# Optimization experiments

Hardware: AMD Instinct MI355X
Metric: run time of the kernel (lower is better)

Reference implementation:

```python
import jax, jax.numpy as jnp
import numpy as np
from jax import lax

DIM = 384
NE = 8
TOPK = 2
HID = 4 * DIM
N, H, W = 32, 32, 32
EPS = 1e-6


def setup_inputs() -> dict:
    key = jax.random.key(0)
    ks = jax.random.split(key, 12)
    s = 0.02
    return {
        "input": jax.random.normal(ks[0], (N, DIM, H, W), dtype=jnp.float32),
        "dw_w": jax.random.normal(ks[1], (DIM, 1, 7, 7), dtype=jnp.float32) * s,
        "dw_b": jnp.zeros((DIM,), dtype=jnp.float32),
        "ln_g": jnp.ones((DIM,), dtype=jnp.float32),
        "ln_b": jnp.zeros((DIM,), dtype=jnp.float32),
        "gate_w": jax.random.normal(ks[2], (NE, DIM), dtype=jnp.float32) * s,
        "w1": jax.random.normal(ks[3], (NE, DIM, HID), dtype=jnp.float32) * s,
        "b1": jnp.zeros((NE, HID), dtype=jnp.float32),
        "w2": jax.random.normal(ks[4], (NE, HID, DIM), dtype=jnp.float32) * s,
        "b2": jnp.zeros((NE, DIM), dtype=jnp.float32),
        "layer_scale": jnp.ones((DIM, 1, 1), dtype=jnp.float32) * 1e-6,
    }


def reference(input, dw_w, dw_b, ln_g, ln_b, gate_w, w1, b1, w2, b2, layer_scale):
    # depthwise 7x7 conv, padding 3, groups=DIM  (NCHW)
    x = lax.conv_general_dilated(
        input, dw_w, window_strides=(1, 1), padding=((3, 3), (3, 3)),
        dimension_numbers=("NCHW", "OIHW", "NCHW"), feature_group_count=DIM,
    ) + dw_b[None, :, None, None]
    # permute to NHWC, layernorm over C with eps=1e-6
    x = jnp.transpose(x, (0, 2, 3, 1))
    mu = jnp.mean(x, axis=-1, keepdims=True)
    var = jnp.mean(jnp.square(x - mu), axis=-1, keepdims=True)
    x = (x - mu) * lax.rsqrt(var + EPS) * ln_g + ln_b

    x_flat = x.reshape(-1, DIM)  # [T, C]
    logits = x_flat @ gate_w.T   # [T, NE]
    topv, topi = lax.top_k(logits, TOPK)
    weights = jax.nn.softmax(topv, axis=-1)  # [T, K]

    # combine: out[t] = sum_e gate_e[t] * Expert_e(x_flat[t]), gate nonzero only for top-k
    out = jnp.zeros_like(x_flat)
    for e in range(NE):
        we = jnp.sum(jnp.where(topi == e, weights, 0.0), axis=-1)  # [T]
        h = jax.nn.gelu(x_flat @ w1[e] + b1[e], approximate=False)
        y = h @ w2[e] + b2[e]
        out = out + y * we[:, None]

    out = out.reshape(N, H, W, DIM)
    out = jnp.transpose(out, (0, 3, 1, 2))  # back to NCHW
    out = layer_scale[None] * out           # [C,1,1] broadcast
    # stochastic_depth prob 0.0 -> identity
    return input + out
```

## Files before the change

### kernel.cpp

```cpp
#include <hip/hip_runtime.h>
#include <hip/hip_bf16.h>
#include <hip/hip_fp8.h>

typedef __attribute__((ext_vector_type(4))) float  f32x4;
typedef __attribute__((ext_vector_type(8))) unsigned short u16x8;
typedef __attribute__((ext_vector_type(4))) unsigned short u16x4;
typedef long long f8x8;

#define DIM 384
#define NE 8
#define HID 1536
#define NB 32
#define HW 1024
#define T_TOK 32768

__device__ __forceinline__ unsigned short f2bf(float f) {
    unsigned int u = __float_as_uint(f);
    u = (u + 0x7fffu + ((u >> 16) & 1u)) >> 16;
    return (unsigned short)u;
}
__device__ __forceinline__ float bf2f(unsigned short u) {
    return __uint_as_float((unsigned int)u << 16);
}
__device__ __forceinline__ unsigned char f2fp8(float f) {
    __hip_fp8_e4m3 h(f);
    return (unsigned char)h.__x;
}

__global__ __launch_bounds__(256) void k_transpose8(const float* __restrict__ src,
                                                    unsigned char* __restrict__ dst,
                                                    int R, int C) {
    int b = blockIdx.x;
    int ctiles = C >> 5;
    int rtiles = R >> 5;
    int ct = b % ctiles;
    int rt = (b / ctiles) % rtiles;
    int e  = b / (ctiles * rtiles);
    __shared__ float t[32][33];
    int tid = threadIdx.x;
    const float* s = src + (size_t)e * R * C;
    unsigned char* d = dst + (size_t)e * C * R;
#pragma unroll
    for (int k = 0; k < 4; ++k) {
        int idx = k * 256 + tid;
        int rr = idx >> 5, cc = idx & 31;
        t[rr][cc] = s[(size_t)(rt * 32 + rr) * C + ct * 32 + cc];
    }
    __syncthreads();
    int cc = tid >> 3, r4 = tid & 7;
    unsigned int pk = 0;
#pragma unroll
    for (int i = 0; i < 4; ++i)
        pk |= (unsigned int)f2fp8(t[r4 * 4 + i][cc]) << (8 * i);
    *(unsigned int*)&d[(size_t)(ct * 32 + cc) * R + rt * 32 + r4 * 4] = pk;
}

__global__ __launch_bounds__(256) void k_conv(const float* __restrict__ in,
                                              const float* __restrict__ dw_w,
                                              const float* __restrict__ dw_b,
                                              float* __restrict__ xconv) {
    int nc = blockIdx.x;
    int c = nc % DIM;
    __shared__ float tile[38 * 38];
    __shared__ float wt[49];
    const float* plane = in + (size_t)nc * HW;
    int tid = threadIdx.x;
    if (tid < 49) wt[tid] = dw_w[c * 49 + tid];
    for (int idx = tid; idx < 38 * 38; idx += 256) {
        int ty = idx / 38, tx = idx % 38;
        int ih = ty - 3, iw = tx - 3;
        float v = 0.f;
        if ((unsigned)ih < 32u && (unsigned)iw < 32u) v = plane[ih * 32 + iw];
        tile[idx] = v;
    }
    __syncthreads();
    float bias = dw_b[c];
    int w = tid & 31, h0 = (tid >> 5) << 2;
    float acc[4] = {bias, bias, bias, bias};
#pragma unroll
    for (int iy = 0; iy < 10; ++iy) {
        float r[7];
#pragma unroll
        for (int dx = 0; dx < 7; ++dx) r[dx] = tile[(h0 + iy) * 38 + w + dx];
#pragma unroll
        for (int o = 0; o < 4; ++o) {
            int dy = iy - o;
            if (dy >= 0 && dy < 7) {
                float a = 0.f;
#pragma unroll
                for (int dx = 0; dx < 7; ++dx) a += r[dx] * wt[dy * 7 + dx];
                acc[o] += a;
            }
        }
    }
    float* outp = xconv + (size_t)nc * HW;
#pragma unroll
    for (int o = 0; o < 4; ++o) outp[(h0 + o) * 32 + w] = acc[o];
}

__global__ __launch_bounds__(256) void k_ln_gate(const float* __restrict__ xconv,
                                                 const float* __restrict__ ln_g,
                                                 const float* __restrict__ ln_b,
                                                 const float* __restrict__ gate_w,
                                                 unsigned char* __restrict__ lnout,
                                                 int* __restrict__ lists,
                                                 float* __restrict__ wgts,
                                                 int* __restrict__ counts) {
    __shared__ float xs[32][385];
    __shared__ float gw[8][384];
    __shared__ float gls[384], bls[384];
    __shared__ int hcnt[8], hbase[8];
    __shared__ int lexp[32][2];
    __shared__ int lpos[32][2];
    __shared__ float lw[32][2];

    int b = blockIdx.x;
    int n = b >> 5;
    int hw0 = (b & 31) << 5;
    int tid = threadIdx.x;

    for (int i = tid; i < 384; i += 256) { gls[i] = ln_g[i]; bls[i] = ln_b[i]; }
    for (int i = tid; i < 8 * 384; i += 256) gw[i / 384][i % 384] = gate_w[i];
    if (tid < 8) hcnt[tid] = 0;

    const float* base = xconv + (size_t)n * DIM * HW + hw0;
#pragma unroll
    for (int k = 0; k < 48; ++k) {
        int idx = k * 256 + tid;
        int c = idx >> 5, j = idx & 31;
        xs[j][c] = base[(size_t)c * HW + j];
    }
    __syncthreads();

    int tok = tid >> 3, jj = tid & 7;
    float sum = 0.f, sq = 0.f;
#pragma unroll
    for (int k = 0; k < 48; ++k) {
        float v = xs[tok][jj + 8 * k];
        sum += v; sq += v * v;
    }
#pragma unroll
    for (int m = 1; m < 8; m <<= 1) { sum += __shfl_xor(sum, m); sq += __shfl_xor(sq, m); }
    float mu = sum * (1.f / 384.f);
    float var = sq * (1.f / 384.f) - mu * mu;
    float rstd = rsqrtf(var + 1e-6f);

    int tglob = n * HW + hw0 + tok;
    float p[8] = {0, 0, 0, 0, 0, 0, 0, 0};
#pragma unroll
    for (int k = 0; k < 48; ++k) {
        int c = jj + 8 * k;
        float v = (xs[tok][c] - mu) * rstd * gls[c] + bls[c];
        lnout[(size_t)tglob * DIM + c] = f2fp8(v);
#pragma unroll
        for (int e = 0; e < 8; ++e) p[e] += v * gw[e][c];
    }
#pragma unroll
    for (int e = 0; e < 8; ++e)
#pragma unroll
        for (int m = 1; m < 8; m <<= 1) p[e] += __shfl_xor(p[e], m);

    if (jj == 0) {
        int i0 = 0; float v0 = p[0];
#pragma unroll
        for (int e = 1; e < 8; ++e) if (p[e] > v0) { v0 = p[e]; i0 = e; }
        int i1 = -1; float v1 = -1e30f;
#pragma unroll
        for (int e = 0; e < 8; ++e) if (e != i0 && p[e] > v1) { v1 = p[e]; i1 = e; }
        float w0 = 1.f / (1.f + __expf(v1 - v0));
        float w1 = 1.f - w0;
        lexp[tok][0] = i0; lexp[tok][1] = i1;
        lw[tok][0] = w0;  lw[tok][1] = w1;
        lpos[tok][0] = atomicAdd(&hcnt[i0], 1);
        lpos[tok][1] = atomicAdd(&hcnt[i1], 1);
    }
    __syncthreads();
    if (tid < 8) hbase[tid] = atomicAdd(&counts[tid], hcnt[tid]);
    __syncthreads();
    if (jj == 0) {
#pragma unroll
        for (int s = 0; s < 2; ++s) {
            int e = lexp[tok][s];
            int pos = hbase[e] + lpos[tok][s];
            lists[e * T_TOK + pos] = (tglob << 1) | s;
            wgts[e * T_TOK + pos] = lw[tok][s];
        }
    }
}

__global__ __launch_bounds__(256, 3) void k_moe(const unsigned char* __restrict__ ln,
                                                const unsigned char* __restrict__ w1t,
                                                const unsigned char* __restrict__ w2t,
                                                const float* __restrict__ b1,
                                                const float* __restrict__ b2,
                                                const int* __restrict__ lists,
                                                const float* __restrict__ wgts,
                                                const int* __restrict__ counts,
                                                unsigned short* __restrict__ y0,
                                                unsigned short* __restrict__ y1) {
    int e    = blockIdx.x & 7;
    int tile = blockIdx.x >> 3;
    int cnt = counts[e];
    if (tile * 64 >= cnt) return;

    __shared__ unsigned char X[64][400];
    __shared__ unsigned char Hs[2][64][136];
    __shared__ int   ents[64];
    __shared__ float wrow[64];

    int tid = threadIdx.x;
    if (tid < 64) {
        int idx = tile * 64 + tid;
        if (idx < cnt) { ents[tid] = lists[e * T_TOK + idx]; wrow[tid] = wgts[e * T_TOK + idx]; }
        else           { ents[tid] = -1;                     wrow[tid] = 0.f; }
    }
    __syncthreads();

    {
        int row = tid >> 2, q = tid & 3;
        int ent = ents[row];
        int tok = (ent < 0) ? 0 : (ent >> 1);
        const u16x8* src = (const u16x8*)(ln + (size_t)tok * DIM);
#pragma unroll
        for (int r = 0; r < 6; ++r)
            *(u16x8*)&X[row][(q + r * 4) * 16] = __builtin_nontemporal_load(&src[q + r * 4]);
    }
    __syncthreads();

    int wid = tid >> 6;
    int lane = tid & 63;
    int lr = lane & 15;
    int lq = lane >> 4;

    const unsigned char* pw1 = w1t + ((size_t)e * HID + wid * 32 + lr) * DIM + lq * 8;
    const unsigned char* pw2 = w2t + ((size_t)e * DIM + wid * 96 + lr) * HID + lq * 8;

    f32x4 Yacc[6][4] = {};

    for (int hc = 0; hc < 12; ++hc) {
        int buf = hc & 1;
        const unsigned char* q1 = pw1 + (size_t)hc * 128 * DIM;
        f32x4 bv0 = *(const f32x4*)&b1[e * HID + hc * 128 + wid * 32 + lq * 4];
        f32x4 bv1 = *(const f32x4*)&b1[e * HID + hc * 128 + wid * 32 + 16 + lq * 4];
        f32x4 Hf[4][2];
#pragma unroll
        for (int m = 0; m < 4; ++m) { Hf[m][0] = bv0; Hf[m][1] = bv1; }
        __builtin_amdgcn_s_setprio(1);
#pragma unroll
        for (int k = 0; k < 12; ++k) {
            f8x8 w0 = *(const f8x8*)(q1 + k * 32);
            f8x8 w1f = *(const f8x8*)(q1 + 16 * DIM + k * 32);
            f8x8 a0 = *(const f8x8*)&X[ 0 + lr][k * 32 + lq * 8];
            f8x8 a1 = *(const f8x8*)&X[16 + lr][k * 32 + lq * 8];
            f8x8 a2 = *(const f8x8*)&X[32 + lr][k * 32 + lq * 8];
            f8x8 a3 = *(const f8x8*)&X[48 + lr][k * 32 + lq * 8];
            Hf[0][0] = __builtin_amdgcn_mfma_f32_16x16x32_fp8_fp8(w0, a0, Hf[0][0], 0, 0, 0);
            Hf[1][0] = __builtin_amdgcn_mfma_f32_16x16x32_fp8_fp8(w0, a1, Hf[1][0], 0, 0, 0);
            Hf[2][0] = __builtin_amdgcn_mfma_f32_16x16x32_fp8_fp8(w0, a2, Hf[2][0], 0, 0, 0);
            Hf[3][0] = __builtin_amdgcn_mfma_f32_16x16x32_fp8_fp8(w0, a3, Hf[3][0], 0, 0, 0);
            Hf[0][1] = __builtin_amdgcn_mfma_f32_16x16x32_fp8_fp8(w1f, a0, Hf[0][1], 0, 0, 0);
            Hf[1][1] = __builtin_amdgcn_mfma_f32_16x16x32_fp8_fp8(w1f, a1, Hf[1][1], 0, 0, 0);
            Hf[2][1] = __builtin_amdgcn_mfma_f32_16x16x32_fp8_fp8(w1f, a2, Hf[2][1], 0, 0, 0);
            Hf[3][1] = __builtin_amdgcn_mfma_f32_16x16x32_fp8_fp8(w1f, a3, Hf[3][1], 0, 0, 0);
        }
        __builtin_amdgcn_s_setprio(0);
#pragma unroll
        for (int nj = 0; nj < 2; ++nj) {
#pragma unroll
            for (int m = 0; m < 4; ++m) {
                unsigned int pk = 0;
#pragma unroll
                for (int r = 0; r < 4; ++r) {
                    float v = Hf[m][nj][r];
                    float zz = v * fmaf(v * v, -0.07135481627f, -1.5957691216f);
                    float g = v * __builtin_amdgcn_rcpf(1.f + __expf(zz));
                    pk |= (unsigned int)f2fp8(g) << (8 * r);
                }
                *(unsigned int*)&Hs[buf][m * 16 + lr][wid * 32 + nj * 16 + lq * 4] = pk;
            }
        }
        asm volatile("s_waitcnt lgkmcnt(0)" ::: "memory");
        __builtin_amdgcn_s_barrier();
        __builtin_amdgcn_sched_barrier(0);
        const unsigned char* q2 = pw2 + hc * 128;
        __builtin_amdgcn_s_setprio(1);
#pragma unroll
        for (int k2 = 0; k2 < 4; ++k2) {
            f8x8 h0 = *(const f8x8*)&Hs[buf][ 0 + lr][k2 * 32 + lq * 8];
            f8x8 h1 = *(const f8x8*)&Hs[buf][16 + lr][k2 * 32 + lq * 8];
            f8x8 h2 = *(const f8x8*)&Hs[buf][32 + lr][k2 * 32 + lq * 8];
            f8x8 h3 = *(const f8x8*)&Hs[buf][48 + lr][k2 * 32 + lq * 8];
#pragma unroll
            for (int nj = 0; nj < 6; ++nj) {
                f8x8 wf = *(const f8x8*)(q2 + (size_t)nj * 16 * HID + k2 * 32);
                Yacc[nj][0] = __builtin_amdgcn_mfma_f32_16x16x32_fp8_fp8(wf, h0, Yacc[nj][0], 0, 0, 0);
                Yacc[nj][1] = __builtin_amdgcn_mfma_f32_16x16x32_fp8_fp8(wf, h1, Yacc[nj][1], 0, 0, 0);
                Yacc[nj][2] = __builtin_amdgcn_mfma_f32_16x16x32_fp8_fp8(wf, h2, Yacc[nj][2], 0, 0, 0);
                Yacc[nj][3] = __builtin_amdgcn_mfma_f32_16x16x32_fp8_fp8(wf, h3, Yacc[nj][3], 0, 0, 0);
            }
        }
        __builtin_amdgcn_s_setprio(0);
    }

    f32x4 b2v[6];
#pragma unroll
    for (int nj = 0; nj < 6; ++nj)
        b2v[nj] = *(const f32x4*)&b2[e * DIM + wid * 96 + nj * 16 + lq * 4];
#pragma unroll
    for (int m = 0; m < 4; ++m) {
        int row = m * 16 + lr;
        int ent = ents[row];
        if (ent >= 0) {
            float wv = wrow[row];
            int tok = ent >> 1;
            unsigned short* yb = (ent & 1) ? y1 : y0;
#pragma unroll
            for (int nj = 0; nj < 6; ++nj) {
                u16x4 pk;
#pragma unroll
                for (int r = 0; r < 4; ++r)
                    pk[r] = f2bf((Yacc[nj][m][r] + b2v[nj][r]) * wv);
                *(u16x4*)(yb + (size_t)tok * DIM + wid * 96 + nj * 16 + lq * 4) = pk;
            }
        }
    }
}

__global__ __launch_bounds__(256) void k_final(const float* __restrict__ input,
                                               const float* __restrict__ ls,
                                               const unsigned short* __restrict__ y0,
                                               const unsigned short* __restrict__ y1,
                                               float* __restrict__ out) {
    int b = blockIdx.x;
    int ct = b % 12;
    int hwt = (b / 12) % 32;
    int n = b / (12 * 32);
    int c0 = ct * 32, hw0 = hwt * 32;
    __shared__ float t[32][33];
    int tid = threadIdx.x;
    int t0 = n * HW + hw0;
#pragma unroll
    for (int k = 0; k < 2; ++k) {
        int idx = k * 256 + tid;
        int tl = idx >> 4, pr = idx & 15;
        size_t o = (size_t)(t0 + tl) * DIM + c0 + pr * 2;
        unsigned int a = *(const unsigned int*)(y0 + o);
        unsigned int c = *(const unsigned int*)(y1 + o);
        t[tl][pr * 2]     = bf2f((unsigned short)a) + bf2f((unsigned short)c);
        t[tl][pr * 2 + 1] = bf2f((unsigned short)(a >> 16)) + bf2f((unsigned short)(c >> 16));
    }
    __syncthreads();
#pragma unroll
    for (int k = 0; k < 4; ++k) {
        int idx = k * 256 + tid;
        int cl = idx >> 5, j = idx & 31;
        size_t o = ((size_t)n * DIM + c0 + cl) * HW + hw0 + j;
        out[o] = input[o] + ls[c0 + cl] * t[j][cl];
    }
}

extern "C" void kernel_launch(void* const* d_in, const int* in_sizes, int n_in,
                              void* d_out, int out_size, void* d_ws, size_t ws_size,
                              hipStream_t stream) {
    const float* input  = (const float*)d_in[0];
    const float* dw_w   = (const float*)d_in[1];
    const float* dw_b   = (const float*)d_in[2];
    const float* ln_g   = (const float*)d_in[3];
    const float* ln_b   = (const float*)d_in[4];
    const float* gate_w = (const float*)d_in[5];
    const float* w1     = (const float*)d_in[6];
    const float* b1     = (const float*)d_in[7];
    const float* w2     = (const float*)d_in[8];
    const float* b2     = (const float*)d_in[9];
    const float* lscale = (const float*)d_in[10];

    const size_t SZ_PLANE = (size_t)NB * DIM * HW * 4;
    const size_t SZ_YBF   = (size_t)T_TOK * DIM * 2;
    const size_t SZ_LNB   = (size_t)T_TOK * DIM;
    const size_t SZ_W1    = (size_t)NE * DIM * HID;
    char* ws = (char*)d_ws;
    float* xconv = (float*)(ws + 0);
    unsigned short* y0 = (unsigned short*)(ws + 0);
    unsigned short* y1 = (unsigned short*)(ws + SZ_YBF);
    unsigned char* lnb = (unsigned char*)(ws + SZ_PLANE);
    unsigned char* w1t = (unsigned char*)(ws + SZ_PLANE + SZ_LNB);
    unsigned char* w2t = (unsigned char*)(ws + SZ_PLANE + SZ_LNB + SZ_W1);
    int*   lists  = (int*)(ws + SZ_PLANE + SZ_LNB + 2 * SZ_W1);
    float* wgt    = (float*)(ws + SZ_PLANE + SZ_LNB + 2 * SZ_W1 + 1048576);
    int*   counts = (int*)(ws + SZ_PLANE + SZ_LNB + 2 * SZ_W1 + 2 * 1048576);
    const size_t needed = SZ_PLANE + SZ_LNB + 2 * SZ_W1 + 2 * 1048576 + 256;
    if (ws_size < needed) return;

    hipMemsetAsync(counts, 0, 32, stream);
    k_transpose8<<<8 * 12 * 48, 256, 0, stream>>>(w1, w1t, DIM, HID);
    k_transpose8<<<8 * 48 * 12, 256, 0, stream>>>(w2, w2t, HID, DIM);
    k_conv<<<NB * DIM, 256, 0, stream>>>(input, dw_w, dw_b, xconv);
    k_ln_gate<<<T_TOK / 32, 256, 0, stream>>>(xconv, ln_g, ln_b, gate_w, lnb, lists, wgt, counts);
    k_moe<<<NE * 512, 256, 0, stream>>>(lnb, w1t, w2t, b1, b2, lists, wgt, counts, y0, y1);
    k_final<<<NB * 32 * 12, 256, 0, stream>>>(input, lscale, y0, y1, (float*)d_out);
}
```

Measured before the change: 485.2 us.

## Restructure MoE kernel into larger hidden chunks with register-prefetched W1 fragments

The MoE kernel now walks the hidden dimension in 4 chunks of 384 instead of 12 chunks of 128. Each wave computes three 32-column slices per chunk with all 12 K-steps of W1 fragments preloaded into registers, and a single enlarged H buffer replaces the double buffer, which adds a second barrier per chunk. This cuts the barrier count and lengthens the second GEMM's inner loop, but raises register use, so launch bounds drop from 3 to 2 blocks per CU. FP8 packing also switches to the hardware packed-convert builtin where available.

```diff
diff --git a/kernel.cpp b/kernel.cpp
--- a/kernel.cpp
+++ b/kernel.cpp
@@ -25,6 +25,20 @@
 __device__ __forceinline__ unsigned char f2fp8(float f) {
     __hip_fp8_e4m3 h(f);
     return (unsigned char)h.__x;
+}
+__device__ __forceinline__ float gelu_f(float v) {
+    float zz = v * fmaf(v * v, -0.07135481627f, -1.5957691216f);
+    return v * __builtin_amdgcn_rcpf(1.f + __expf(zz));
+}
+__device__ __forceinline__ unsigned int pk4_fp8(float a, float b, float c, float d) {
+#if __has_builtin(__builtin_amdgcn_cvt_pk_fp8_f32)
+    int v = __builtin_amdgcn_cvt_pk_fp8_f32(a, b, 0, false);
+    v = __builtin_amdgcn_cvt_pk_fp8_f32(c, d, v, true);
+    return (unsigned int)v;
+#else
+    return (unsigned int)f2fp8(a) | ((unsigned int)f2fp8(b) << 8) |
+           ((unsigned int)f2fp8(c) << 16) | ((unsigned int)f2fp8(d) << 24);
+#endif
 }
 
 __global__ __launch_bounds__(256) void k_transpose8(const float* __restrict__ src,
@@ -48,10 +62,8 @@
     }
     __syncthreads();
     int cc = tid >> 3, r4 = tid & 7;
-    unsigned int pk = 0;
-#pragma unroll
-    for (int i = 0; i < 4; ++i)
-        pk |= (unsigned int)f2fp8(t[r4 * 4 + i][cc]) << (8 * i);
+    unsigned int pk = pk4_fp8(t[r4 * 4 + 0][cc], t[r4 * 4 + 1][cc],
+                              t[r4 * 4 + 2][cc], t[r4 * 4 + 3][cc]);
     *(unsigned int*)&d[(size_t)(ct * 32 + cc) * R + rt * 32 + r4 * 4] = pk;
 }
 
@@ -188,7 +200,7 @@
     }
 }
 
-__global__ __launch_bounds__(256, 3) void k_moe(const unsigned char* __restrict__ ln,
+__global__ __launch_bounds__(256, 2) void k_moe(const unsigned char* __restrict__ ln,
                                                 const unsigned char* __restrict__ w1t,
                                                 const unsigned char* __restrict__ w2t,
                                                 const float* __restrict__ b1,
@@ -204,7 +216,7 @@
     if (tile * 64 >= cnt) return;
 
     __shared__ unsigned char X[64][400];
-    __shared__ unsigned char Hs[2][64][136];
+    __shared__ unsigned char Hs[64][392];
     __shared__ int   ents[64];
     __shared__ float wrow[64];
 
@@ -227,69 +239,69 @@
     }
     __syncthreads();
 
-    int wid = tid >> 6;
+    int w    = tid >> 6;
     int lane = tid & 63;
     int lr = lane & 15;
     int lq = lane >> 4;
 
-    const unsigned char* pw1 = w1t + ((size_t)e * HID + wid * 32 + lr) * DIM + lq * 8;
-    const unsigned char* pw2 = w2t + ((size_t)e * DIM + wid * 96 + lr) * HID + lq * 8;
-
     f32x4 Yacc[6][4] = {};
 
-    for (int hc = 0; hc < 12; ++hc) {
-        int buf = hc & 1;
-        const unsigned char* q1 = pw1 + (size_t)hc * 128 * DIM;
-        f32x4 bv0 = *(const f32x4*)&b1[e * HID + hc * 128 + wid * 32 + lq * 4];
-        f32x4 bv1 = *(const f32x4*)&b1[e * HID + hc * 128 + wid * 32 + 16 + lq * 4];
-        f32x4 Hf[4][2];
-#pragma unroll
-        for (int m = 0; m < 4; ++m) { Hf[m][0] = bv0; Hf[m][1] = bv1; }
+    for (int hc = 0; hc < 4; ++hc) {
         __builtin_amdgcn_s_setprio(1);
 #pragma unroll
-        for (int k = 0; k < 12; ++k) {
-            f8x8 w0 = *(const f8x8*)(q1 + k * 32);
-            f8x8 w1f = *(const f8x8*)(q1 + 16 * DIM + k * 32);
-            f8x8 a0 = *(const f8x8*)&X[ 0 + lr][k * 32 + lq * 8];
-            f8x8 a1 = *(const f8x8*)&X[16 + lr][k * 32 + lq * 8];
-            f8x8 a2 = *(const f8x8*)&X[32 + lr][k * 32 + lq * 8];
-            f8x8 a3 = *(const f8x8*)&X[48 + lr][k * 32 + lq * 8];
-            Hf[0][0] = __builtin_amdgcn_mfma_f32_16x16x32_fp8_fp8(w0, a0, Hf[0][0], 0, 0, 0);
-            Hf[1][0] = __builtin_amdgcn_mfma_f32_16x16x32_fp8_fp8(w0, a1, Hf[1][0], 0, 0, 0);
-            Hf[2][0] = __builtin_amdgcn_mfma_f32_16x16x32_fp8_fp8(w0, a2, Hf[2][0], 0, 0, 0);
-            Hf[3][0] = __builtin_amdgcn_mfma_f32_16x16x32_fp8_fp8(w0, a3, Hf[3][0], 0, 0, 0);
-            Hf[0][1] = __builtin_amdgcn_mfma_f32_16x16x32_fp8_fp8(w1f, a0, Hf[0][1], 0, 0, 0);
-            Hf[1][1] = __builtin_amdgcn_mfma_f32_16x16x32_fp8_fp8(w1f, a1, Hf[1][1], 0, 0, 0);
-            Hf[2][1] = __builtin_amdgcn_mfma_f32_16x16x32_fp8_fp8(w1f, a2, Hf[2][1], 0, 0, 0);
-            Hf[3][1] = __builtin_amdgcn_mfma_f32_16x16x32_fp8_fp8(w1f, a3, Hf[3][1], 0, 0, 0);
+        for (int s = 0; s < 3; ++s) {
+            int hb = hc * 384 + w * 96 + s * 32;
+            const unsigned char* pa = w1t + ((size_t)e * HID + hb + lr) * DIM + lq * 8;
+            f8x8 wa[2][12];
+#pragma unroll
+            for (int nj = 0; nj < 2; ++nj)
+#pragma unroll
+                for (int k = 0; k < 12; ++k)
+                    wa[nj][k] = *(const f8x8*)(pa + (size_t)nj * 16 * DIM + k * 32);
+            f32x4 bv0 = *(const f32x4*)&b1[e * HID + hb + lq * 4];
+            f32x4 bv1 = *(const f32x4*)&b1[e * HID + hb + 16 + lq * 4];
+            f32x4 Hacc[2][4];
+#pragma unroll
+            for (int m = 0; m < 4; ++m) { Hacc[0][m] = bv0; Hacc[1][m] = bv1; }
+#pragma unroll
+            for (int k = 0; k < 12; ++k) {
+                f8x8 a0 = *(const f8x8*)&X[ 0 + lr][k * 32 + lq * 8];
+                f8x8 a1 = *(const f8x8*)&X[16 + lr][k * 32 + lq * 8];
+                f8x8 a2 = *(const f8x8*)&X[32 + lr][k * 32 + lq * 8];
+                f8x8 a3 = *(const f8x8*)&X[48 + lr][k * 32 + lq * 8];
+                Hacc[0][0] = __builtin_amdgcn_mfma_f32_16x16x32_fp8_fp8(wa[0][k], a0, Hacc[0][0], 0, 0, 0);
+                Hacc[0][1] = __builtin_amdgcn_mfma_f32_16x16x32_fp8_fp8(wa[0][k], a1, Hacc[0][1], 0, 0, 0);
+                Hacc[0][2] = __builtin_amdgcn_mfma_f32_16x16x32_fp8_fp8(wa[0][k], a2, Hacc[0][2], 0, 0, 0);
+                Hacc[0][3] = __builtin_amdgcn_mfma_f32_16x16x32_fp8_fp8(wa[0][k], a3, Hacc[0][3], 0, 0, 0);
+                Hacc[1][0] = __builtin_amdgcn_mfma_f32_16x16x32_fp8_fp8(wa[1][k], a0, Hacc[1][0], 0, 0, 0);
+                Hacc[1][1] = __builtin_amdgcn_mfma_f32_16x16x32_fp8_fp8(wa[1][k], a1, Hacc[1][1], 0, 0, 0);
+                Hacc[1][2] = __builtin_amdgcn_mfma_f32_16x16x32_fp8_fp8(wa[1][k], a2, Hacc[1][2], 0, 0, 0);
+                Hacc[1][3] = __builtin_amdgcn_mfma_f32_16x16x32_fp8_fp8(wa[1][k], a3, Hacc[1][3], 0, 0, 0);
+            }
+#pragma unroll
+            for (int nj = 0; nj < 2; ++nj) {
+                int col = w * 96 + s * 32 + nj * 16 + lq * 4;
+#pragma unroll
+                for (int m = 0; m < 4; ++m) {
+                    f32x4 hv = Hacc[nj][m];
+                    unsigned int pk = pk4_fp8(gelu_f(hv[0]), gelu_f(hv[1]),
+                                              gelu_f(hv[2]), gelu_f(hv[3]));
+                    *(unsigned int*)&Hs[m * 16 + lr][col] = pk;
+                }
+            }
         }
         __builtin_amdgcn_s_setprio(0);
-#pragma unroll
-        for (int nj = 0; nj < 2; ++nj) {
-#pragma unroll
-            for (int m = 0; m < 4; ++m) {
-                unsigned int pk = 0;
-#pragma unroll
-                for (int r = 0; r < 4; ++r) {
-                    float v = Hf[m][nj][r];
-                    float zz = v * fmaf(v * v, -0.07135481627f, -1.5957691216f);
-                    float g = v * __builtin_amdgcn_rcpf(1.f + __expf(zz));
-                    pk |= (unsigned int)f2fp8(g) << (8 * r);
-                }
-                *(unsigned int*)&Hs[buf][m * 16 + lr][wid * 32 + nj * 16 + lq * 4] = pk;
-            }
-        }
         asm volatile("s_waitcnt lgkmcnt(0)" ::: "memory");
         __builtin_amdgcn_s_barrier();
         __builtin_amdgcn_sched_barrier(0);
-        const unsigned char* q2 = pw2 + hc * 128;
+        const unsigned char* q2 = w2t + ((size_t)e * DIM + w * 96 + lr) * HID + hc * 384 + lq * 8;
         __builtin_amdgcn_s_setprio(1);
 #pragma unroll
-        for (int k2 = 0; k2 < 4; ++k2) {
-            f8x8 h0 = *(const f8x8*)&Hs[buf][ 0 + lr][k2 * 32 + lq * 8];
-            f8x8 h1 = *(const f8x8*)&Hs[buf][16 + lr][k2 * 32 + lq * 8];
-            f8x8 h2 = *(const f8x8*)&Hs[buf][32 + lr][k2 * 32 + lq * 8];
-            f8x8 h3 = *(const f8x8*)&Hs[buf][48 + lr][k2 * 32 + lq * 8];
+        for (int k2 = 0; k2 < 12; ++k2) {
+            f8x8 h0 = *(const f8x8*)&Hs[ 0 + lr][k2 * 32 + lq * 8];
+            f8x8 h1 = *(const f8x8*)&Hs[16 + lr][k2 * 32 + lq * 8];
+            f8x8 h2 = *(const f8x8*)&Hs[32 + lr][k2 * 32 + lq * 8];
+            f8x8 h3 = *(const f8x8*)&Hs[48 + lr][k2 * 32 + lq * 8];
 #pragma unroll
             for (int nj = 0; nj < 6; ++nj) {
                 f8x8 wf = *(const f8x8*)(q2 + (size_t)nj * 16 * HID + k2 * 32);
@@ -300,12 +312,15 @@
             }
         }
         __builtin_amdgcn_s_setprio(0);
+        asm volatile("s_waitcnt lgkmcnt(0)" ::: "memory");
+        __builtin_amdgcn_s_barrier();
+        __builtin_amdgcn_sched_barrier(0);
     }
 
     f32x4 b2v[6];
 #pragma unroll
     for (int nj = 0; nj < 6; ++nj)
-        b2v[nj] = *(const f32x4*)&b2[e * DIM + wid * 96 + nj * 16 + lq * 4];
+        b2v[nj] = *(const f32x4*)&b2[e * DIM + w * 96 + nj * 16 + lq * 4];
 #pragma unroll
     for (int m = 0; m < 4; ++m) {
         int row = m * 16 + lr;
@@ -320,7 +335,7 @@
 #pragma unroll
                 for (int r = 0; r < 4; ++r)
                     pk[r] = f2bf((Yacc[nj][m][r] + b2v[nj][r]) * wv);
-                *(u16x4*)(yb + (size_t)tok * DIM + wid * 96 + nj * 16 + lq * 4) = pk;
+                *(u16x4*)(yb + (size_t)tok * DIM + w * 96 + nj * 16 + lq * 4) = pk;
             }
         }
     }
```

Result: slower. 542.3 us (+11.8%).
